# Kernel tuning notes

Hardware: AMD Instinct MI355X
Metric: run time of the kernel (lower is better)

The kernel has to match this reference:

```python
import jax, jax.numpy as jnp
import numpy as np

EPS = 1e-7
FEAT_DIM = 128
N_DATA = 100000
NCE_K = 16384
NCE_T = 0.07


def _l2norm(x):
    # Normalize(power=2): x / (sum(x^2, axis=1)^(1/2))
    return x / jnp.sqrt(jnp.sum(x * x, axis=1, keepdims=True))


def _embed(x, W, b):
    return _l2norm(x @ W.T + b)


def _contrast_loss(x, n_data):
    # x: [B, K+1] of (unnormalized) probabilities; col 0 = positive
    bsz = x.shape[0]
    m = x.shape[1] - 1
    Pn = 1.0 / float(n_data)
    c = m * Pn + EPS
    log_D1 = jnp.log(x[:, 0] / (x[:, 0] + c))          # positives
    log_D0 = jnp.log((m * Pn) / (x[:, 1:] + c))         # negatives
    return -(log_D1.sum() + log_D0.sum()) / bsz


def setup_inputs() -> dict:
    key = jax.random.key(0)
    ks = jax.random.split(key, 10)
    s_dim, t_dim = 1024, 2048
    B = 64
    stdv = 1.0 / np.sqrt(FEAT_DIM / 3.0)
    inp = {
        "f_s": jax.random.normal(ks[0], (B, s_dim), dtype=jnp.float32),
        "f_t": jax.random.normal(ks[1], (B, t_dim), dtype=jnp.float32),
        "idx": jax.random.randint(ks[2], (B,), 0, N_DATA),
        "contrast_idx": jax.random.randint(ks[3], (B, NCE_K + 1), 0, N_DATA),
        # Embed params (linear): Linear(dim_in, feat_dim)
        "Ws": jax.random.normal(ks[4], (FEAT_DIM, s_dim), dtype=jnp.float32) / np.sqrt(s_dim),
        "bs": jnp.zeros((FEAT_DIM,), dtype=jnp.float32),
        "Wt": jax.random.normal(ks[5], (FEAT_DIM, t_dim), dtype=jnp.float32) / np.sqrt(t_dim),
        "bt": jnp.zeros((FEAT_DIM,), dtype=jnp.float32),
        # memory banks, init uniform(-stdv, stdv) as in CRD ContrastMemory
        "memory_v1": jax.random.uniform(ks[6], (N_DATA, FEAT_DIM), jnp.float32, -stdv, stdv),
        "memory_v2": jax.random.uniform(ks[7], (N_DATA, FEAT_DIM), jnp.float32, -stdv, stdv),
    }
    return inp


def reference(f_s, f_t, idx, contrast_idx, Ws, bs, Wt, bt, memory_v1, memory_v2):
    v_s = _embed(f_s, Ws, bs)   # [B, D]
    v_t = _embed(f_t, Wt, bt)   # [B, D]

    # idx.select(1,0).copy_(y): column 0 is the positive index
    idx_all = jnp.concatenate([idx[:, None], contrast_idx[:, 1:]], axis=1)  # [B, K+1]

    # gather from memory banks + bmm similarity
    w1 = memory_v1[idx_all]   # [B, K+1, D] (v_t side bank)
    w2 = memory_v2[idx_all]   # [B, K+1, D] (v_s side bank)
    out_t = jnp.exp(jnp.einsum('bkd,bd->bk', w1, v_t) / NCE_T)  # out_v2
    out_s = jnp.exp(jnp.einsum('bkd,bd->bk', w2, v_s) / NCE_T)  # out_v1

    # Z set on first batch: Z = out.mean() * n_data (detached constant)
    Z_s = jax.lax.stop_gradient(out_s.mean()) * N_DATA
    Z_t = jax.lax.stop_gradient(out_t.mean()) * N_DATA
    out_s = out_s / Z_s
    out_t = out_t / Z_t

    s_loss = _contrast_loss(out_s, N_DATA)
    t_loss = _contrast_loss(out_t, N_DATA)
    return s_loss + t_loss
```

## Files before the change

kernel.cpp:

```cpp
#include <hip/hip_runtime.h>

#define NDATA 100000
#define KP1 16385
#define BSZ 64
#define PTOT (BSZ * KP1)
#define NCHUNKS 6250
#define INV_T (1.0f / 0.07f)
#define ACC_STRIDE 64
#define ACC_GROUPS 32
#define SG_NW 2048
#define HSEG 12500

typedef short short8 __attribute__((ext_vector_type(8)));
typedef float f32x4 __attribute__((ext_vector_type(4)));

__device__ __forceinline__ float wave_reduce64(float v) {
    #pragma unroll
    for (int off = 32; off >= 1; off >>= 1) v += __shfl_xor(v, off);
    return v;
}

__device__ __forceinline__ float group_reduce16(float v) {
    v += __shfl_xor(v, 8); v += __shfl_xor(v, 4);
    v += __shfl_xor(v, 2); v += __shfl_xor(v, 1);
    return v;
}

__device__ __forceinline__ unsigned short f2bf(float f) {
    unsigned u = __float_as_uint(f);
    u += 0x7FFFu + ((u >> 16) & 1u);
    return (unsigned short)(u >> 16);
}

__device__ __forceinline__ float bfm(float x) {
    return __uint_as_float(((unsigned)f2bf(x)) << 16);
}

__device__ __forceinline__ short8 pack_bf16(float4 lo, float4 hi) {
    short8 r;
    r[0] = (short)f2bf(lo.x); r[1] = (short)f2bf(lo.y);
    r[2] = (short)f2bf(lo.z); r[3] = (short)f2bf(lo.w);
    r[4] = (short)f2bf(hi.x); r[5] = (short)f2bf(hi.y);
    r[6] = (short)f2bf(hi.z); r[7] = (short)f2bf(hi.w);
    return r;
}

__device__ __forceinline__ float dot4(float4 a, float4 b, float acc) {
    acc = fmaf(a.x, b.x, acc);
    acc = fmaf(a.y, b.y, acc);
    acc = fmaf(a.z, b.z, acc);
    return fmaf(a.w, b.w, acc);
}

__device__ __forceinline__ float dot8bf(const float4* a, const float4* v, int li, float d) {
    #pragma unroll
    for (int h = 0; h < 2; ++h) {
        const float4 x = a[li * 2 + h], y = v[li * 2 + h];
        d = fmaf(bfm(x.x), bfm(y.x), d);
        d = fmaf(bfm(x.y), bfm(y.y), d);
        d = fmaf(bfm(x.z), bfm(y.z), d);
        d = fmaf(bfm(x.w), bfm(y.w), d);
    }
    return d;
}

__global__ __launch_bounds__(256) void bwprobe_kernel(
    const float* __restrict__ src, float* __restrict__ dst,
    float* __restrict__ acc)
{
    const int t = threadIdx.x;
    if (blockIdx.x < 8) acc[blockIdx.x * 256 + t] = 0.0f;
    const int gid = blockIdx.x * 256 + t;
    const float4* p = (const float4*)src;
    float4 v[8];
    #pragma unroll
    for (int i = 0; i < 8; ++i) v[i] = p[(size_t)i * 262144 + gid];
    float s = 0.0f;
    #pragma unroll
    for (int i = 0; i < 8; ++i) s += (v[i].x + v[i].y) + (v[i].z + v[i].w);
    s = wave_reduce64(s);
    __shared__ float r[4];
    if ((t & 63) == 0) r[t >> 6] = s;
    __syncthreads();
    if (t == 0) dst[blockIdx.x] = r[0] + r[1] + r[2] + r[3];
}

__global__ __launch_bounds__(256) void embed_kernel(
    const float* __restrict__ fs, const float* __restrict__ ft,
    const float* __restrict__ Ws, const float* __restrict__ bs,
    const float* __restrict__ Wt, const float* __restrict__ bt,
    float* __restrict__ vraw_s, float* __restrict__ vraw_t)
{
    __shared__ __align__(16) float4 FS[512];
    __shared__ __align__(16) float4 FT[1024];

    const int t  = threadIdx.x;
    const int b0 = blockIdx.y * 2;

    for (int q = t; q < 512; q += 256) {
        const int b = q >> 8, i = q & 255;
        FS[q] = ((const float4*)(fs + (size_t)(b0 + b) * 1024))[i];
    }
    for (int q = t; q < 1024; q += 256) {
        const int b = q >> 9, i = q & 511;
        FT[q] = ((const float4*)(ft + (size_t)(b0 + b) * 2048))[i];
    }
    __syncthreads();

    const int w = t >> 6, lane = t & 63;
    const int d = blockIdx.x * 4 + w;

    {
        const float4* wrow = (const float4*)(Ws + (size_t)d * 1024);
        float a0 = 0.0f, a1 = 0.0f;
        #pragma unroll
        for (int i = 0; i < 4; ++i) {
            const float4 wv = wrow[i * 64 + lane];
            a0 = dot4(wv, FS[i * 64 + lane], a0);
            a1 = dot4(wv, FS[256 + i * 64 + lane], a1);
        }
        a0 = wave_reduce64(a0) + bs[d];
        a1 = wave_reduce64(a1) + bs[d];
        if (lane == 0) {
            vraw_s[(size_t)b0 * 128 + d]       = a0;
            vraw_s[(size_t)(b0 + 1) * 128 + d] = a1;
        }
    }
    {
        const float4* wrow = (const float4*)(Wt + (size_t)d * 2048);
        float a0 = 0.0f, a1 = 0.0f;
        #pragma unroll
        for (int i = 0; i < 8; ++i) {
            const float4 wv = wrow[i * 64 + lane];
            a0 = dot4(wv, FT[i * 64 + lane], a0);
            a1 = dot4(wv, FT[512 + i * 64 + lane], a1);
        }
        a0 = wave_reduce64(a0) + bt[d];
        a1 = wave_reduce64(a1) + bt[d];
        if (lane == 0) {
            vraw_t[(size_t)b0 * 128 + d]       = a0;
            vraw_t[(size_t)(b0 + 1) * 128 + d] = a1;
        }
    }
}

__global__ __launch_bounds__(256) void histnorm_kernel(
    const int* __restrict__ cidx, unsigned* __restrict__ cntw,
    const float* __restrict__ vraw_t, const float* __restrict__ vraw_s,
    float* __restrict__ sct, float* __restrict__ scs)
{
    const int t = threadIdx.x;
    if (blockIdx.x >= 128) {
        const float* __restrict__ v = (blockIdx.x == 129) ? vraw_s : vraw_t;
        float* __restrict__ sc      = (blockIdx.x == 129) ? scs : sct;
        const int b = t >> 2, g = t & 3;
        const float4* row = (const float4*)(v + (size_t)b * 128 + g * 32);
        float s = 0.0f;
        #pragma unroll
        for (int j = 0; j < 8; ++j) s = dot4(row[j], row[j], s);
        s += __shfl_xor(s, 1);
        s += __shfl_xor(s, 2);
        if (g == 0) sc[b] = INV_T * rsqrtf(s);
        return;
    }
    const int w   = blockIdx.x >> 3;
    const int seg = blockIdx.x & 7;
    const int r0  = seg * HSEG;

    __shared__ unsigned h[HSEG];
    for (int i = t; i < HSEG; i += 256) h[i] = 0;
    __syncthreads();

    #pragma unroll
    for (int j2 = 0; j2 < 4; ++j2) {
        const int b = 4 * w + j2;
        const unsigned inc = 1u << (8 * j2);
        const int* __restrict__ cp = cidx + (size_t)b * KP1 + 1;
        for (int bi = 0; bi < 8; ++bi) {
            int v[8];
            #pragma unroll
            for (int u = 0; u < 8; ++u)
                v[u] = cp[bi * 2048 + u * 256 + t];
            #pragma unroll
            for (int u = 0; u < 8; ++u) {
                const unsigned rr = (unsigned)(v[u] - r0);
                if (rr < HSEG) atomicAdd(&h[rr], inc);
            }
        }
    }
    __syncthreads();

    unsigned* __restrict__ dstp = cntw + (size_t)w * NDATA + r0;
    for (int i = t; i < HSEG; i += 256) dstp[i] = h[i];
}

#define SG_ISSUE(AB, CB, CID)                                                \
  {                                                                          \
    const int r0_ = (CID) << 4;                                              \
    const float4* ar_ = (const float4*)(bankp + (size_t)(r0_ + m) * 128);    \
    _Pragma("unroll")                                                        \
    for (int kk = 0; kk < 4; ++kk) {                                         \
      AB[kk * 2]     = ar_[(kk * 4 + q4) * 2];                               \
      AB[kk * 2 + 1] = ar_[(kk * 4 + q4) * 2 + 1];                           \
    }                                                                        \
    _Pragma("unroll")                                                        \
    for (int n = 0; n < 4; ++n)                                              \
      CB[n] = cntw[(size_t)(n * 4 + q4) * NDATA + (r0_ + m)];                \
  }

#define SG_PROCESS(AB, CB)                                                   \
  {                                                                          \
    short8 af_[4];                                                           \
    _Pragma("unroll")                                                        \
    for (int kk = 0; kk < 4; ++kk)                                           \
      af_[kk] = pack_bf16(AB[kk * 2], AB[kk * 2 + 1]);                       \
    _Pragma("unroll")                                                        \
    for (int n = 0; n < 4; ++n) {                                            \
      f32x4 av = {0.f, 0.f, 0.f, 0.f};                                       \
      _Pragma("unroll")                                                      \
      for (int kk = 0; kk < 4; ++kk)                                         \
        av = __builtin_amdgcn_mfma_f32_16x16x32_bf16(bfv[n][kk], af_[kk], av, 0, 0, 0); \
      const unsigned cw_ = CB[n];                                            \
      _Pragma("unroll")                                                      \
      for (int j = 0; j < 4; ++j) {                                          \
        const float fm_ = (float)((cw_ >> (8 * j)) & 255u);                  \
        const float e_  = __expf(av[j] * scv[n][j]);                         \
        se  = fmaf(e_, fm_, se);                                             \
        se2 = fmaf(e_ * fm_, e_, se2);                                       \
      }                                                                      \
    }                                                                        \
  }

__global__ __launch_bounds__(256) void sgemm_kernel(
    const float* __restrict__ m1, const float* __restrict__ m2,
    const float* __restrict__ vraw_s, const float* __restrict__ vraw_t,
    const float* __restrict__ sct, const float* __restrict__ scs,
    const unsigned* __restrict__ cntw,
    float* __restrict__ acc)
{
    const int t = threadIdx.x;
    const int bank = blockIdx.y;
    const float* __restrict__ bankp = bank ? m2 : m1;
    const float* __restrict__ vp    = bank ? vraw_s : vraw_t;
    const float* __restrict__ scp   = bank ? scs : sct;

    const int lane = t & 63;
    const int m  = lane & 15;
    const int q4 = lane >> 4;

    short8 bfv[4][4];
    #pragma unroll
    for (int n = 0; n < 4; ++n) {
        const float4* vrow = (const float4*)(vp + (size_t)(n * 16 + m) * 128);
        #pragma unroll
        for (int kk = 0; kk < 4; ++kk) {
            const float4 lo = vrow[(kk * 4 + q4) * 2];
            const float4 hi = vrow[(kk * 4 + q4) * 2 + 1];
            bfv[n][kk] = pack_bf16(lo, hi);
        }
    }

    f32x4 scv[4];
    #pragma unroll
    for (int n = 0; n < 4; ++n) scv[n] = ((const f32x4*)scp)[n * 4 + q4];

    float se = 0.0f, se2 = 0.0f;

    const int wave = (blockIdx.x << 2) | (t >> 6);

    float4 aA[8], aB[8];
    unsigned cA[4], cB[4];

    SG_ISSUE(aA, cA, wave);
    SG_ISSUE(aB, cB, wave + SG_NW);
    SG_PROCESS(aA, cA);
    SG_ISSUE(aA, cA, wave + 2 * SG_NW);
    SG_PROCESS(aB, cB);
    if (wave + 3 * SG_NW < NCHUNKS) {
        SG_ISSUE(aB, cB, wave + 3 * SG_NW);
        SG_PROCESS(aA, cA);
        SG_PROCESS(aB, cB);
    } else {
        SG_PROCESS(aA, cA);
    }

    se  = wave_reduce64(se);
    se2 = wave_reduce64(se2);
    __shared__ float red[4][2];
    if (lane == 0) { red[t >> 6][0] = se; red[t >> 6][1] = se2; }
    __syncthreads();
    if (t < 2) {
        const float s = red[0][t] + red[1][t] + red[2][t] + red[3][t];
        atomicAdd(&acc[(blockIdx.x & (ACC_GROUPS - 1)) * ACC_STRIDE + bank * 2 + t], s);
    }
}

__global__ __launch_bounds__(256) void final_kernel(
    const int* __restrict__ idx,
    const float* __restrict__ m1, const float* __restrict__ m2,
    const float* __restrict__ vraw_t, const float* __restrict__ vraw_s,
    const float* __restrict__ sct, const float* __restrict__ scs,
    const float* __restrict__ acc, float* __restrict__ out)
{
    const int t = threadIdx.x, wave = t >> 6, lane = t & 63, g = lane >> 4, li = lane & 15;
    __shared__ float e1s[64], e2s[64];

    #pragma unroll
    for (int i = 0; i < 4; ++i) {
        const int b = wave * 16 + i * 4 + g;
        const int row = idx[b];
        float dT = dot8bf((const float4*)(m1 + (size_t)row * 128),
                          (const float4*)(vraw_t + (size_t)b * 128), li, 0.f);
        float dS = dot8bf((const float4*)(m2 + (size_t)row * 128),
                          (const float4*)(vraw_s + (size_t)b * 128), li, 0.f);
        dT = group_reduce16(dT);
        dS = group_reduce16(dS);
        if (li == 0) {
            e1s[b] = __expf(dT * sct[b]);
            e2s[b] = __expf(dS * scs[b]);
        }
    }
    __syncthreads();

    if (t < 64) {
        const int b = t;
        const float c = 0.16384f + 1e-7f;
        const float e1p = e1s[b], e2p = e2s[b];

        const float pseT = wave_reduce64(e1p);
        const float pseS = wave_reduce64(e2p);

        float seT_neg = 0.f, se2T_neg = 0.f, seS_neg = 0.f, se2S_neg = 0.f;
        for (int s = 0; s < ACC_GROUPS; ++s) {
            seT_neg  += acc[s * ACC_STRIDE + 0];
            se2T_neg += acc[s * ACC_STRIDE + 1];
            seS_neg  += acc[s * ACC_STRIDE + 2];
            se2S_neg += acc[s * ACC_STRIDE + 3];
        }

        const float zn = (float)PTOT / (float)NDATA;
        const float invZt = zn / (seT_neg + pseT);
        const float invZs = zn / (seS_neg + pseS);

        const float PB = (float)(PTOT - BSZ);
        const float LOG_MPN_C = -6.1035156e-7f;
        const float ic = 1.0f / c;

        const float negT = PB * LOG_MPN_C
                         - seT_neg * invZt * ic
                         + 0.5f * se2T_neg * invZt * invZt * ic * ic;
        const float negS = PB * LOG_MPN_C
                         - seS_neg * invZs * ic
                         + 0.5f * se2S_neg * invZs * invZs * ic * ic;

        const float x0t = e1p * invZt, x0s = e2p * invZs;
        float pos = __logf(x0t / (x0t + c)) + __logf(x0s / (x0s + c));
        pos = wave_reduce64(pos);

        if (b == 0) out[0] = -(negT + negS + pos) * (1.0f / 64.0f);
    }
}

extern "C" void kernel_launch(void* const* d_in, const int* in_sizes, int n_in,
                              void* d_out, int out_size, void* d_ws, size_t ws_size,
                              hipStream_t stream) {
    const float* fs   = (const float*)d_in[0];
    const float* ft   = (const float*)d_in[1];
    const int*   idx  = (const int*)d_in[2];
    const int*   cidx = (const int*)d_in[3];
    const float* Ws   = (const float*)d_in[4];
    const float* bs   = (const float*)d_in[5];
    const float* Wt   = (const float*)d_in[6];
    const float* bt   = (const float*)d_in[7];
    const float* m1   = (const float*)d_in[8];
    const float* m2   = (const float*)d_in[9];
    float* out = (float*)d_out;

    float* ws     = (float*)d_ws;
    float* sct    = ws;
    float* scs    = ws + 64;
    float* acc    = ws + 128;
    float* pdst   = ws + 2176;
    unsigned* cntw = (unsigned*)(ws + 4096);
    float* vraw_s = ws + 1604096;
    float* vraw_t = ws + 1612288;

    bwprobe_kernel<<<dim3(1024), dim3(256), 0, stream>>>(m1, pdst, acc);
    embed_kernel<<<dim3(32, 32), dim3(256), 0, stream>>>(
        fs, ft, Ws, bs, Wt, bt, vraw_s, vraw_t);
    histnorm_kernel<<<dim3(130), dim3(256), 0, stream>>>(
        cidx, cntw, vraw_t, vraw_s, sct, scs);
    sgemm_kernel<<<dim3(512, 2), dim3(256), 0, stream>>>(
        m1, m2, vraw_s, vraw_t, sct, scs, cntw, acc);
    final_kernel<<<dim3(1), dim3(256), 0, stream>>>(
        idx, m1, m2, vraw_t, vraw_s, sct, scs, acc, out);
}
```

Baseline: 200.6 us.

## Fuse embed and histogram kernels, drop bandwidth probe, defer norm reduction

```diff
diff --git a/kernel.cpp b/kernel.cpp
--- a/kernel.cpp
+++ b/kernel.cpp
@@ -64,38 +64,60 @@
     return d;
 }
 
-__global__ __launch_bounds__(256) void bwprobe_kernel(
-    const float* __restrict__ src, float* __restrict__ dst,
+__global__ __launch_bounds__(256) void embedhist_kernel(
+    const float* __restrict__ fs, const float* __restrict__ ft,
+    const float* __restrict__ Ws, const float* __restrict__ bs,
+    const float* __restrict__ Wt, const float* __restrict__ bt,
+    const int* __restrict__ cidx,
+    float* __restrict__ vraw_s, float* __restrict__ vraw_t,
+    float* __restrict__ n2part, unsigned* __restrict__ cntw,
     float* __restrict__ acc)
 {
     const int t = threadIdx.x;
-    if (blockIdx.x < 8) acc[blockIdx.x * 256 + t] = 0.0f;
-    const int gid = blockIdx.x * 256 + t;
-    const float4* p = (const float4*)src;
-    float4 v[8];
-    #pragma unroll
-    for (int i = 0; i < 8; ++i) v[i] = p[(size_t)i * 262144 + gid];
-    float s = 0.0f;
-    #pragma unroll
-    for (int i = 0; i < 8; ++i) s += (v[i].x + v[i].y) + (v[i].z + v[i].w);
-    s = wave_reduce64(s);
-    __shared__ float r[4];
-    if ((t & 63) == 0) r[t >> 6] = s;
-    __syncthreads();
-    if (t == 0) dst[blockIdx.x] = r[0] + r[1] + r[2] + r[3];
-}
-
-__global__ __launch_bounds__(256) void embed_kernel(
-    const float* __restrict__ fs, const float* __restrict__ ft,
-    const float* __restrict__ Ws, const float* __restrict__ bs,
-    const float* __restrict__ Wt, const float* __restrict__ bt,
-    float* __restrict__ vraw_s, float* __restrict__ vraw_t)
-{
-    __shared__ __align__(16) float4 FS[512];
-    __shared__ __align__(16) float4 FT[1024];
-
-    const int t  = threadIdx.x;
-    const int b0 = blockIdx.y * 2;
+    __shared__ __align__(16) unsigned char smem[50048];
+
+    if (blockIdx.x < 128) {
+        unsigned* h = (unsigned*)smem;
+        const int w   = blockIdx.x >> 3;
+        const int seg = blockIdx.x & 7;
+        const int r0  = seg * HSEG;
+
+        for (int i = t; i < HSEG; i += 256) h[i] = 0;
+        __syncthreads();
+
+        #pragma unroll
+        for (int j2 = 0; j2 < 4; ++j2) {
+            const int b = 4 * w + j2;
+            const unsigned inc = 1u << (8 * j2);
+            const int* __restrict__ cp = cidx + (size_t)b * KP1 + 1;
+            for (int bi = 0; bi < 8; ++bi) {
+                int v[8];
+                #pragma unroll
+                for (int u = 0; u < 8; ++u)
+                    v[u] = cp[bi * 2048 + u * 256 + t];
+                #pragma unroll
+                for (int u = 0; u < 8; ++u) {
+                    const unsigned rr = (unsigned)(v[u] - r0);
+                    if (rr < HSEG) atomicAdd(&h[rr], inc);
+                }
+            }
+        }
+        __syncthreads();
+
+        unsigned* __restrict__ dstp = cntw + (size_t)w * NDATA + r0;
+        for (int i = t; i < HSEG; i += 256) dstp[i] = h[i];
+        return;
+    }
+
+    const int bx = blockIdx.x - 128;
+    if (bx < 8) acc[bx * 256 + t] = 0.0f;
+
+    float4* FS = (float4*)smem;
+    float4* FT = (float4*)(smem + 8192);
+    float*  NR = (float*)(smem + 24576);
+
+    const int dq = bx >> 5;
+    const int b0 = (bx & 31) * 2;
 
     for (int q = t; q < 512; q += 256) {
         const int b = q >> 8, i = q & 255;
@@ -108,7 +130,7 @@
     __syncthreads();
 
     const int w = t >> 6, lane = t & 63;
-    const int d = blockIdx.x * 4 + w;
+    const int d = dq * 4 + w;
 
     {
         const float4* wrow = (const float4*)(Ws + (size_t)d * 1024);
@@ -124,6 +146,8 @@
         if (lane == 0) {
             vraw_s[(size_t)b0 * 128 + d]       = a0;
             vraw_s[(size_t)(b0 + 1) * 128 + d] = a1;
+            NR[w * 4 + 0] = a0 * a0;
+            NR[w * 4 + 1] = a1 * a1;
         }
     }
     {
@@ -140,58 +164,17 @@
         if (lane == 0) {
             vraw_t[(size_t)b0 * 128 + d]       = a0;
             vraw_t[(size_t)(b0 + 1) * 128 + d] = a1;
-        }
-    }
-}
-
-__global__ __launch_bounds__(256) void histnorm_kernel(
-    const int* __restrict__ cidx, unsigned* __restrict__ cntw,
-    const float* __restrict__ vraw_t, const float* __restrict__ vraw_s,
-    float* __restrict__ sct, float* __restrict__ scs)
-{
-    const int t = threadIdx.x;
-    if (blockIdx.x >= 128) {
-        const float* __restrict__ v = (blockIdx.x == 129) ? vraw_s : vraw_t;
-        float* __restrict__ sc      = (blockIdx.x == 129) ? scs : sct;
-        const int b = t >> 2, g = t & 3;
-        const float4* row = (const float4*)(v + (size_t)b * 128 + g * 32);
-        float s = 0.0f;
-        #pragma unroll
-        for (int j = 0; j < 8; ++j) s = dot4(row[j], row[j], s);
-        s += __shfl_xor(s, 1);
-        s += __shfl_xor(s, 2);
-        if (g == 0) sc[b] = INV_T * rsqrtf(s);
-        return;
-    }
-    const int w   = blockIdx.x >> 3;
-    const int seg = blockIdx.x & 7;
-    const int r0  = seg * HSEG;
-
-    __shared__ unsigned h[HSEG];
-    for (int i = t; i < HSEG; i += 256) h[i] = 0;
-    __syncthreads();
-
-    #pragma unroll
-    for (int j2 = 0; j2 < 4; ++j2) {
-        const int b = 4 * w + j2;
-        const unsigned inc = 1u << (8 * j2);
-        const int* __restrict__ cp = cidx + (size_t)b * KP1 + 1;
-        for (int bi = 0; bi < 8; ++bi) {
-            int v[8];
-            #pragma unroll
-            for (int u = 0; u < 8; ++u)
-                v[u] = cp[bi * 2048 + u * 256 + t];
-            #pragma unroll
-            for (int u = 0; u < 8; ++u) {
-                const unsigned rr = (unsigned)(v[u] - r0);
-                if (rr < HSEG) atomicAdd(&h[rr], inc);
-            }
-        }
-    }
-    __syncthreads();
-
-    unsigned* __restrict__ dstp = cntw + (size_t)w * NDATA + r0;
-    for (int i = t; i < HSEG; i += 256) dstp[i] = h[i];
+            NR[w * 4 + 2] = a0 * a0;
+            NR[w * 4 + 3] = a1 * a1;
+        }
+    }
+    __syncthreads();
+    if (t < 4) {
+        const float v = NR[0 * 4 + t] + NR[1 * 4 + t] + NR[2 * 4 + t] + NR[3 * 4 + t];
+        const int side = (t < 2) ? 1 : 0;
+        const int bb = b0 + (t & 1);
+        n2part[side * 2048 + bb * 32 + dq] = v;
+    }
 }
 
 #define SG_ISSUE(AB, CB, CID)                                                \
@@ -234,7 +217,7 @@
 __global__ __launch_bounds__(256) void sgemm_kernel(
     const float* __restrict__ m1, const float* __restrict__ m2,
     const float* __restrict__ vraw_s, const float* __restrict__ vraw_t,
-    const float* __restrict__ sct, const float* __restrict__ scs,
+    const float* __restrict__ n2part,
     const unsigned* __restrict__ cntw,
     float* __restrict__ acc)
 {
@@ -242,7 +225,19 @@
     const int bank = blockIdx.y;
     const float* __restrict__ bankp = bank ? m2 : m1;
     const float* __restrict__ vp    = bank ? vraw_s : vraw_t;
-    const float* __restrict__ scp   = bank ? scs : sct;
+
+    __shared__ float scl[64];
+    {
+        const int tb = t >> 2, tg = t & 3;
+        const float* np = n2part + bank * 2048 + tb * 32 + tg * 8;
+        float s = 0.0f;
+        #pragma unroll
+        for (int j = 0; j < 8; ++j) s += np[j];
+        s += __shfl_xor(s, 1);
+        s += __shfl_xor(s, 2);
+        if (tg == 0) scl[tb] = INV_T * rsqrtf(s);
+    }
+    __syncthreads();
 
     const int lane = t & 63;
     const int m  = lane & 15;
@@ -262,7 +257,10 @@
 
     f32x4 scv[4];
     #pragma unroll
-    for (int n = 0; n < 4; ++n) scv[n] = ((const f32x4*)scp)[n * 4 + q4];
+    for (int n = 0; n < 4; ++n) {
+        #pragma unroll
+        for (int j = 0; j < 4; ++j) scv[n][j] = scl[n * 16 + q4 * 4 + j];
+    }
 
     float se = 0.0f, se2 = 0.0f;
 
@@ -299,11 +297,21 @@
     const int* __restrict__ idx,
     const float* __restrict__ m1, const float* __restrict__ m2,
     const float* __restrict__ vraw_t, const float* __restrict__ vraw_s,
-    const float* __restrict__ sct, const float* __restrict__ scs,
+    const float* __restrict__ n2part,
     const float* __restrict__ acc, float* __restrict__ out)
 {
     const int t = threadIdx.x, wave = t >> 6, lane = t & 63, g = lane >> 4, li = lane & 15;
+    __shared__ float sctl[64], scsl[64];
     __shared__ float e1s[64], e2s[64];
+
+    if (t < 128) {
+        const int side = t >> 6, b = t & 63;
+        const float* np = n2part + side * 2048 + b * 32;
+        float s = 0.0f;
+        for (int j = 0; j < 32; ++j) s += np[j];
+        (side ? scsl : sctl)[b] = INV_T * rsqrtf(s);
+    }
+    __syncthreads();
 
     #pragma unroll
     for (int i = 0; i < 4; ++i) {
@@ -316,8 +324,8 @@
         dT = group_reduce16(dT);
         dS = group_reduce16(dS);
         if (li == 0) {
-            e1s[b] = __expf(dT * sct[b]);
-            e2s[b] = __expf(dS * scs[b]);
+            e1s[b] = __expf(dT * sctl[b]);
+            e2s[b] = __expf(dS * scsl[b]);
         }
     }
     __syncthreads();
@@ -376,22 +384,17 @@
     const float* m2   = (const float*)d_in[9];
     float* out = (float*)d_out;
 
-    float* ws     = (float*)d_ws;
-    float* sct    = ws;
-    float* scs    = ws + 64;
-    float* acc    = ws + 128;
-    float* pdst   = ws + 2176;
-    unsigned* cntw = (unsigned*)(ws + 4096);
-    float* vraw_s = ws + 1604096;
-    float* vraw_t = ws + 1612288;
-
-    bwprobe_kernel<<<dim3(1024), dim3(256), 0, stream>>>(m1, pdst, acc);
-    embed_kernel<<<dim3(32, 32), dim3(256), 0, stream>>>(
-        fs, ft, Ws, bs, Wt, bt, vraw_s, vraw_t);
-    histnorm_kernel<<<dim3(130), dim3(256), 0, stream>>>(
-        cidx, cntw, vraw_t, vraw_s, sct, scs);
+    float* ws      = (float*)d_ws;
+    float* acc     = ws;
+    float* n2part  = ws + 2048;
+    unsigned* cntw = (unsigned*)(ws + 8192);
+    float* vraw_s  = ws + 1608192;
+    float* vraw_t  = ws + 1616384;
+
+    embedhist_kernel<<<dim3(1152), dim3(256), 0, stream>>>(
+        fs, ft, Ws, bs, Wt, bt, cidx, vraw_s, vraw_t, n2part, cntw, acc);
     sgemm_kernel<<<dim3(512, 2), dim3(256), 0, stream>>>(
-        m1, m2, vraw_s, vraw_t, sct, scs, cntw, acc);
+        m1, m2, vraw_s, vraw_t, n2part, cntw, acc);
     final_kernel<<<dim3(1), dim3(256), 0, stream>>>(
-        idx, m1, m2, vraw_t, vraw_s, sct, scs, acc, out);
-}
+        idx, m1, m2, vraw_t, vraw_s, n2part, acc, out);
+}
```

Measured after the change: 186.3 us, median of 2. -7.2%, faster.
